# Optimization experiments

Measured on AMD Instinct MI355X. Metric: run time of the kernel, lower is better.

Reference implementation:

```python
import jax, jax.numpy as jnp
import numpy as np

C_S = 384; C_Z = 256; HD = 16; NH = 12; NQ = 4; NV = 8; L = 512
WC = float(np.sqrt(2.0 / (9.0 * NQ)))
WL = float(np.sqrt(1.0 / 3.0))


def quat2rot(q):
    # q: [L,4] -> R: [L,3,3] (normalized quaternion to rotation matrix)
    q = q / jnp.linalg.norm(q, axis=-1, keepdims=True)
    w, x, y, z = q[..., 0], q[..., 1], q[..., 2], q[..., 3]
    R = jnp.stack([
        1 - 2 * (y * y + z * z), 2 * (x * y - w * z), 2 * (x * z + w * y),
        2 * (x * y + w * z), 1 - 2 * (x * x + z * z), 2 * (y * z - w * x),
        2 * (x * z - w * y), 2 * (y * z + w * x), 1 - 2 * (x * x + y * y)
    ], axis=-1)
    return R.reshape(q.shape[:-1] + (3, 3))


def _layer_norm(x, g, b, eps=1e-5):
    m = x.mean(-1, keepdims=True)
    v = x.var(-1, keepdims=True)
    return (x - m) / jnp.sqrt(v + eps) * g + b


def setup_inputs() -> dict:
    key = jax.random.key(0)
    ks = jax.random.split(key, 20)
    f32 = jnp.float32
    def w(k, shape, fan_in):
        return (jax.random.normal(k, shape) / np.sqrt(fan_in)).astype(f32)
    shid = NH * (C_Z + HD + NV * 3 + NV)  # 3648
    return {
        "s": jax.random.normal(ks[0], (1, L, C_S), f32),
        "z": jax.random.normal(ks[1], (1, L, L, C_Z), f32),
        "quat_tns": jax.random.normal(ks[2], (1, L, 4), f32),
        "trsl_tns": jax.random.normal(ks[3], (1, L, 3), f32),
        "Wq": w(ks[4], (C_S, NH * HD), C_S),
        "Wk": w(ks[5], (C_S, NH * HD), C_S),
        "Wv": w(ks[6], (C_S, NH * HD), C_S),
        "Wqp": w(ks[7], (C_S, NH * NQ * 3), C_S),
        "Wkp": w(ks[8], (C_S, NH * NQ * 3), C_S),
        "Wvp": w(ks[9], (C_S, NH * NV * 3), C_S),
        "Wb": w(ks[10], (C_Z, NH), C_Z),
        "Ws": w(ks[11], (shid, C_S), shid),
        "bs": jnp.zeros((C_S,), f32),
        "scale": jnp.full((NH,), np.log(np.e - 1.0), f32),
        "g1": jnp.ones((C_S,), f32), "b1": jnp.zeros((C_S,), f32),
        "Wm1": w(ks[12], (C_S, C_S), C_S), "bm1": jnp.zeros((C_S,), f32),
        "Wm2": w(ks[13], (C_S, C_S), C_S), "bm2": jnp.zeros((C_S,), f32),
        "Wm3": w(ks[14], (C_S, C_S), C_S), "bm3": jnp.zeros((C_S,), f32),
        "g2": jnp.ones((C_S,), f32), "b2": jnp.zeros((C_S,), f32),
    }


def reference(s, z, quat_tns, trsl_tns, Wq, Wk, Wv, Wqp, Wkp, Wvp, Wb, Ws, bs,
              scale, g1, b1, Wm1, bm1, Wm2, bm2, Wm3, bm3, g2, b2):
    N, Lr, _ = s.shape
    q = (s @ Wq).reshape(N, Lr, NH, HD)
    k = (s @ Wk).reshape(N, Lr, NH, HD)
    v = (s @ Wv).reshape(N, Lr, NH, HD)
    qp = (s @ Wqp).reshape(N, Lr, NH, NQ, 3)
    kp = (s @ Wkp).reshape(N, Lr, NH, NQ, 3)
    vp = (s @ Wvp).reshape(N, Lr, NH, NV, 3)
    b = z @ Wb                                   # [N,L,L,H]
    R = quat2rot(quat_tns[0])[None]              # [1,L,3,3]
    t = trsl_tns[:, :, None, None, :]            # [1,L,1,1,3]

    def fwd_trans(x):                            # global frame: R x + t
        return jnp.einsum('nlij,nlhpj->nlhpi', R, x) + t

    qpp = fwd_trans(qp)                          # [N,L,H,Q,3]
    kpp = fwd_trans(kp)
    vpp = fwd_trans(vp)                          # [N,L,H,V,3]

    # sum over points and coords of squared distances -> [N,L,L,H]
    d2 = jnp.sum((qpp[:, :, None] - kpp[:, None, :]) ** 2, axis=(-1, -2))
    qk = jnp.einsum('nihd,njhd->nijh', q, k) / np.sqrt(HD)
    qkp = 0.5 * WC * jax.nn.softplus(scale)[None, None, None, :] * d2
    a = jax.nn.softmax(WL * (qk + b - qkp), axis=2)  # softmax over keys j

    op = jnp.einsum('nijh,nijc->nihc', a, z)         # [N,L,H,C_Z]
    ov = jnp.einsum('nijh,njhd->nihd', a, v)         # [N,L,H,HD]
    ovp_g = jnp.einsum('nijh,njhp->nihp', a, vpp.reshape(N, Lr, NH, NV * 3))
    ovp_g = ovp_g.reshape(N, Lr, NH, NV, 3)
    # inverse transform: R^T (y - t)
    ovp = jnp.einsum('nlji,nlhvj->nlhvi', R, ovp_g - t)
    ovp_norm = jnp.linalg.norm(ovp, axis=-1)         # [N,L,H,V]

    shid = jnp.concatenate(
        [op, ov, ovp.reshape(N, Lr, NH, NV * 3), ovp_norm], axis=3
    ).reshape(N, Lr, -1)
    s1 = _layer_norm(s + shid @ Ws + bs, g1, b1)
    h = jax.nn.relu(s1 @ Wm1 + bm1)
    h = jax.nn.relu(h @ Wm2 + bm2)
    h = h @ Wm3 + bm3
    return _layer_norm(s1 + h, g2, b2)
```

## Files before the change

### kernel.cpp

```cpp
#include <hip/hip_runtime.h>
#include <math.h>

#define LSEQ 512
#define CS 384
#define CZ 256
#define HD 16
#define NH 12
#define NQ 4
#define NV 8
#define NALL 1152
#define SHID 3648
#define OFF_Q 0
#define OFF_K 192
#define OFF_V 384
#define OFF_QP 576
#define OFF_KP 720
#define OFF_VP 864

#define WC_CONST 0.2357022603955158f
#define WL_CONST 0.5773502691896258f

typedef __attribute__((ext_vector_type(8))) short bf16x8;
typedef __attribute__((ext_vector_type(4))) float f32x4;

__device__ __forceinline__ short f2bf(float f) {
  unsigned u = __builtin_bit_cast(unsigned, f);
  unsigned r = (u + 0x7FFF + ((u >> 16) & 1)) >> 16;
  return (short)r;
}

__global__ void k_prep(const float* quat, const float* trsl, const float* scale,
                       const float* Wb, float* R, float* T, float* CH,
                       unsigned short* WBP) {
  int t = threadIdx.x;
  if (t < LSEQ) {
    float w = quat[t*4+0], x = quat[t*4+1], y = quat[t*4+2], z = quat[t*4+3];
    float inv = 1.0f / sqrtf(w*w + x*x + y*y + z*z);
    w *= inv; x *= inv; y *= inv; z *= inv;
    float* r = R + t*9;
    r[0] = 1.f - 2.f*(y*y + z*z); r[1] = 2.f*(x*y - w*z);       r[2] = 2.f*(x*z + w*y);
    r[3] = 2.f*(x*y + w*z);       r[4] = 1.f - 2.f*(x*x + z*z); r[5] = 2.f*(y*z - w*x);
    r[6] = 2.f*(x*z - w*y);       r[7] = 2.f*(y*z + w*x);       r[8] = 1.f - 2.f*(x*x + y*y);
    T[t*3+0] = trsl[t*3+0]; T[t*3+1] = trsl[t*3+1]; T[t*3+2] = trsl[t*3+2];
  }
  if (t < NH) {
    float sc = scale[t];
    float sp = (sc > 20.f) ? sc : logf(1.f + expf(sc));
    CH[t] = 0.5f * WC_CONST * sp;
  }
  if (t < CZ) {
    #pragma unroll
    for (int h = 0; h < 16; h++)
      WBP[t*16 + h] = (h < NH) ? (unsigned short)f2bf(Wb[t*NH + h]) : (unsigned short)0;
  }
}

__global__ void k_concat(const float* Wq, const float* Wk, const float* Wv,
                         const float* Wqp, const float* Wkp, const float* Wvp,
                         float* Wcat) {
  int idx = blockIdx.x * 256 + threadIdx.x;
  if (idx >= CS * NALL) return;
  int r = idx / NALL, c = idx % NALL;
  float v;
  if (c < 192)       v = Wq [r*192 + c];
  else if (c < 384)  v = Wk [r*192 + (c-192)];
  else if (c < 576)  v = Wv [r*192 + (c-384)];
  else if (c < 720)  v = Wqp[r*144 + (c-576)];
  else if (c < 864)  v = Wkp[r*144 + (c-720)];
  else               v = Wvp[r*288 + (c-864)];
  Wcat[idx] = v;
}

__global__ __launch_bounds__(256) void k_gemm(
    const float* A, const float* B, float* C, const float* bias,
    int K, int lda, int ldb, int ldc, int splitk, int relu, int reluA) {
  int ks = blockIdx.z;
  int Ksub = K / splitk;
  int kbeg = ks * Ksub, kend = kbeg + Ksub;

  __shared__ __align__(16) float As[16][68];
  __shared__ __align__(16) float Bs[16][68];
  int t = threadIdx.x;
  int m0 = blockIdx.y * 64, n0 = blockIdx.x * 64;
  int arow = t >> 2,  akq = (t & 3) * 4;
  int bkk  = t >> 4,  bnq = (t & 15) * 4;
  int ty = (t >> 4) * 4, tx = (t & 15) * 4;
  float acc[4][4];
  #pragma unroll
  for (int r = 0; r < 4; r++)
    #pragma unroll
    for (int c = 0; c < 4; c++) acc[r][c] = 0.f;

  const float* aptr  = A + (long)(m0 + arow) * lda + akq;
  const float* bbase = B + n0 + bnq;
  float4 av = *(const float4*)&aptr[kbeg];
  float4 bv = *(const float4*)&bbase[(long)(kbeg + bkk) * ldb];

  for (int kb = kbeg; kb < kend; kb += 16) {
    float4 a_cur = av, b_cur = bv;
    if (reluA) {
      a_cur.x = fmaxf(a_cur.x, 0.f); a_cur.y = fmaxf(a_cur.y, 0.f);
      a_cur.z = fmaxf(a_cur.z, 0.f); a_cur.w = fmaxf(a_cur.w, 0.f);
    }
    __syncthreads();
    As[akq+0][arow] = a_cur.x; As[akq+1][arow] = a_cur.y;
    As[akq+2][arow] = a_cur.z; As[akq+3][arow] = a_cur.w;
    *(float4*)&Bs[bkk][bnq] = b_cur;
    __syncthreads();
    if (kb + 16 < kend) {
      av = *(const float4*)&aptr[kb + 16];
      bv = *(const float4*)&bbase[(long)(kb + 16 + bkk) * ldb];
    }
    #pragma unroll
    for (int kk = 0; kk < 16; kk++) {
      float4 a4 = *(float4*)&As[kk][ty];
      float4 b4 = *(float4*)&Bs[kk][tx];
      acc[0][0] += a4.x*b4.x; acc[0][1] += a4.x*b4.y; acc[0][2] += a4.x*b4.z; acc[0][3] += a4.x*b4.w;
      acc[1][0] += a4.y*b4.x; acc[1][1] += a4.y*b4.y; acc[1][2] += a4.y*b4.z; acc[1][3] += a4.y*b4.w;
      acc[2][0] += a4.z*b4.x; acc[2][1] += a4.z*b4.y; acc[2][2] += a4.z*b4.z; acc[2][3] += a4.z*b4.w;
      acc[3][0] += a4.w*b4.x; acc[3][1] += a4.w*b4.y; acc[3][2] += a4.w*b4.z; acc[3][3] += a4.w*b4.w;
    }
  }

  if (splitk == 1) {
    #pragma unroll
    for (int r = 0; r < 4; r++) {
      int m = m0 + ty + r;
      #pragma unroll
      for (int c = 0; c < 4; c++) {
        int n = n0 + tx + c;
        float v = acc[r][c] + (bias ? bias[n] : 0.f);
        if (relu) v = fmaxf(v, 0.f);
        C[(long)m * ldc + n] = v;
      }
    }
  } else {
    #pragma unroll
    for (int r = 0; r < 4; r++) {
      int m = m0 + ty + r;
      #pragma unroll
      for (int c = 0; c < 4; c++) {
        int n = n0 + tx + c;
        float v = acc[r][c] + ((ks == 0 && bias) ? bias[n] : 0.f);
        atomicAdd(&C[(long)m * ldc + n], v);
      }
    }
  }
}

__global__ void k_trans(const float* P, const float* R, const float* T,
                        float* QPP, float* KT, float* KPT, float* VBT) {
  int task = blockIdx.y;
  int idx = blockIdx.x * 256 + threadIdx.x;
  if (idx >= LSEQ * NH) return;
  int h = idx / LSEQ, l = idx % LSEQ;
  const float* r = R + l*9;
  float t0 = T[l*3], t1 = T[l*3+1], t2 = T[l*3+2];
  const float* prow = P + (long)l * NALL;
  if (task == 0) {
    #pragma unroll
    for (int pq = 0; pq < NQ; pq++) {
      const float* x = prow + OFF_QP + h*12 + pq*3;
      float a = x[0], b = x[1], c = x[2];
      float* o = QPP + l*144 + h*12 + pq*3;
      o[0] = r[0]*a + r[1]*b + r[2]*c + t0;
      o[1] = r[3]*a + r[4]*b + r[5]*c + t1;
      o[2] = r[6]*a + r[7]*b + r[8]*c + t2;
    }
    #pragma unroll
    for (int d = 0; d < HD; d++)
      KT[(h*HD + d)*LSEQ + l] = prow[OFF_K + h*HD + d];
  } else if (task == 1) {
    #pragma unroll
    for (int pq = 0; pq < NQ; pq++) {
      const float* x = prow + OFF_KP + h*12 + pq*3;
      float a = x[0], b = x[1], c = x[2];
      KPT[(h*12 + pq*3 + 0)*LSEQ + l] = r[0]*a + r[1]*b + r[2]*c + t0;
      KPT[(h*12 + pq*3 + 1)*LSEQ + l] = r[3]*a + r[4]*b + r[5]*c + t1;
      KPT[(h*12 + pq*3 + 2)*LSEQ + l] = r[6]*a + r[7]*b + r[8]*c + t2;
    }
  } else {
    #pragma unroll
    for (int d = 0; d < 16; d++)
      VBT[((long)(h*40 + d))*LSEQ + l] = prow[OFF_V + h*16 + d];
    #pragma unroll
    for (int pv = 0; pv < NV; pv++) {
      const float* x = prow + OFF_VP + h*24 + pv*3;
      float a = x[0], b = x[1], c = x[2];
      VBT[((long)(h*40 + 16 + 3*pv + 0))*LSEQ + l] = r[0]*a + r[1]*b + r[2]*c + t0;
      VBT[((long)(h*40 + 16 + 3*pv + 1))*LSEQ + l] = r[3]*a + r[4]*b + r[5]*c + t1;
      VBT[((long)(h*40 + 16 + 3*pv + 2))*LSEQ + l] = r[6]*a + r[7]*b + r[8]*c + t2;
    }
  }
}

__global__ __launch_bounds__(512) void k_logit(const float* P, const float* QPP,
    const float* KT, const float* KPT, const float* CH, float* LG) {
  int i = blockIdx.x;
  int j = threadIdx.x;
  #pragma unroll
  for (int h = 0; h < NH; h++) {
    float kreg[16];
    #pragma unroll
    for (int d = 0; d < 16; d++) kreg[d] = KT[(h*16 + d)*LSEQ + j];
    float kp[12];
    #pragma unroll
    for (int p = 0; p < 12; p++) kp[p] = KPT[(h*12 + p)*LSEQ + j];
    float ch = CH[h];
    const float* q  = P + (long)i*NALL + OFF_Q + h*HD;
    const float* qp = QPP + i*144 + h*12;
    float dot = 0.f;
    #pragma unroll
    for (int d = 0; d < 16; d++) dot += q[d] * kreg[d];
    float d2 = 0.f;
    #pragma unroll
    for (int p = 0; p < 12; p++) { float dd = qp[p] - kp[p]; d2 += dd*dd; }
    LG[((long)i*NH + h)*LSEQ + j] = WL_CONST * (0.25f*dot - ch*d2);
  }
}

__global__ __launch_bounds__(256) void k_fused(const float* zin,
    const unsigned short* WBP, const float* LG, const float* VBT,
    float* SH, float* OVT, float* SSUM) {
  __shared__ __align__(16) float lgs[NH][264];
  __shared__ __align__(16) float es[NH][68];
  __shared__ float sred[4][NH];
  int i = blockIdx.x, js = blockIdx.y, t = threadIdx.x;
  int jbase = js * 256;
  int w = t >> 6, l = t & 63;
  int r = l & 15, kg = l >> 4;

  const float* lgsrc = LG + (long)i * NH * LSEQ + jbase;
  #pragma unroll
  for (int idx = t; idx < NH*256/4; idx += 256) {
    int h = idx >> 6, q4 = idx & 63;
    *(float4*)&lgs[h][q4*4] = *(const float4*)&lgsrc[h*LSEQ + q4*4];
  }

  bf16x8 bfrag[8];
  #pragma unroll
  for (int kt = 0; kt < 8; kt++)
    #pragma unroll
    for (int jj = 0; jj < 8; jj++)
      bfrag[kt][jj] = (short)WBP[(kt*32 + kg*8 + jj)*16 + r];

  float accop[NH];
  #pragma unroll
  for (int h = 0; h < NH; h++) accop[h] = 0.f;
  int pair0 = t, pair1 = t + 256;
  int h0 = pair0 / 40;
  int h1 = pair1 / 40;
  float accv0 = 0.f, accv1 = 0.f;
  float sparts = 0.f;
  int hh = (r < NH) ? r : 0;

  __syncthreads();

  for (int jt = 0; jt < 256; jt += 64) {
    int j0 = jt + w*16;
    int j0g = jbase + j0;
    const float* zrow = zin + ((long)i*LSEQ + j0g + r)*CZ + kg*8;
    f32x4 acc = {0.f, 0.f, 0.f, 0.f};
    #pragma unroll
    for (int kt = 0; kt < 8; kt++) {
      float4 z0 = *(const float4*)(zrow + kt*32);
      float4 z1 = *(const float4*)(zrow + kt*32 + 4);
      bf16x8 af;
      af[0] = f2bf(z0.x); af[1] = f2bf(z0.y); af[2] = f2bf(z0.z); af[3] = f2bf(z0.w);
      af[4] = f2bf(z1.x); af[5] = f2bf(z1.y); af[6] = f2bf(z1.z); af[7] = f2bf(z1.w);
      acc = __builtin_amdgcn_mfma_f32_16x16x32_bf16(af, bfrag[kt], acc, 0, 0, 0);
    }
    float4 lgv = *(float4*)&lgs[hh][j0 + kg*4];
    float e0 = __expf(lgv.x + WL_CONST*acc[0]);
    float e1 = __expf(lgv.y + WL_CONST*acc[1]);
    float e2 = __expf(lgv.z + WL_CONST*acc[2]);
    float e3 = __expf(lgv.w + WL_CONST*acc[3]);
    if (r < NH) {
      sparts += e0 + e1 + e2 + e3;
      *(float4*)&es[r][w*16 + kg*4] = make_float4(e0, e1, e2, e3);
    }
    __syncthreads();
    const float* zc = zin + ((long)i*LSEQ + jbase + jt)*CZ + t;
    #pragma unroll 4
    for (int jj = 0; jj < 64; jj += 4) {
      float z0 = zc[(jj+0)*CZ], z1 = zc[(jj+1)*CZ];
      float z2 = zc[(jj+2)*CZ], z3 = zc[(jj+3)*CZ];
      #pragma unroll
      for (int h = 0; h < NH; h++) {
        float4 ev = *(float4*)&es[h][jj];
        accop[h] += ev.x*z0 + ev.y*z1 + ev.z*z2 + ev.w*z3;
      }
    }
    {
      const float* vb0 = VBT + ((long)pair0)*LSEQ + jbase + jt;
      #pragma unroll
      for (int jj = 0; jj < 64; jj += 4) {
        float4 vv = *(const float4*)&vb0[jj];
        float4 ev = *(float4*)&es[h0][jj];
        accv0 += vv.x*ev.x + vv.y*ev.y + vv.z*ev.z + vv.w*ev.w;
      }
      if (pair1 < 480) {
        const float* vb1 = VBT + ((long)pair1)*LSEQ + jbase + jt;
        #pragma unroll
        for (int jj = 0; jj < 64; jj += 4) {
          float4 vv = *(const float4*)&vb1[jj];
          float4 ev = *(float4*)&es[h1][jj];
          accv1 += vv.x*ev.x + vv.y*ev.y + vv.z*ev.z + vv.w*ev.w;
        }
      }
    }
    __syncthreads();
  }

  sparts += __shfl_xor(sparts, 16);
  sparts += __shfl_xor(sparts, 32);
  if (l < NH) sred[w][l] = sparts;
  __syncthreads();
  if (t < NH)
    atomicAdd(&SSUM[i*16 + t], sred[0][t] + sred[1][t] + sred[2][t] + sred[3][t]);

  float* sh = SH + (long)i * SHID + t;
  #pragma unroll
  for (int h = 0; h < NH; h++) atomicAdd(&sh[h * 304], accop[h]);
  atomicAdd(&OVT[(long)i*480 + pair0], accv0);
  if (pair1 < 480) atomicAdd(&OVT[(long)i*480 + pair1], accv1);
}

__global__ __launch_bounds__(256) void k_opnorm(const float* SSUM, float* SH) {
  int i = blockIdx.x, t = threadIdx.x;
  float* sh = SH + (long)i * SHID + t;
  #pragma unroll
  for (int h = 0; h < NH; h++) {
    float inv = 1.0f / SSUM[i*16 + h];
    sh[h * 304] *= inv;
  }
}

__global__ void k_ovp(const float* OVT, const float* SSUM, const float* R,
                      const float* T, float* SH) {
  int idx = blockIdx.x * 256 + threadIdx.x;
  if (idx >= LSEQ * NH) return;
  int l = idx / NH, h = idx % NH;
  float inv = 1.0f / SSUM[l*16 + h];
  const float* o = OVT + (long)l*480 + h*40;
  float* sh = SH + (long)l * SHID + h * 304;
  #pragma unroll
  for (int d = 0; d < 16; d++) sh[256 + d] = o[d] * inv;
  const float* r = R + l*9;
  float t0 = T[l*3], t1 = T[l*3+1], t2 = T[l*3+2];
  #pragma unroll
  for (int v = 0; v < NV; v++) {
    float a = o[16+3*v+0]*inv - t0, b = o[16+3*v+1]*inv - t1, c = o[16+3*v+2]*inv - t2;
    float x = r[0]*a + r[3]*b + r[6]*c;
    float y = r[1]*a + r[4]*b + r[7]*c;
    float zz= r[2]*a + r[5]*b + r[8]*c;
    sh[272 + 3*v + 0] = x;
    sh[272 + 3*v + 1] = y;
    sh[272 + 3*v + 2] = zz;
    sh[296 + v] = sqrtf(x*x + y*y + zz*zz);
  }
}

__global__ __launch_bounds__(384) void k_ln(const float* res, const float* y,
                                            const float* g, const float* b, float* out) {
  int l = blockIdx.x, t = threadIdx.x;
  __shared__ float red1[6], red2[6];
  __shared__ float mv[2];
  float x = res[(long)l * CS + t] + y[(long)l * CS + t];
  float s = x, s2 = x * x;
  #pragma unroll
  for (int off = 32; off >= 1; off >>= 1) { s += __shfl_xor(s, off); s2 += __shfl_xor(s2, off); }
  if ((t & 63) == 0) { red1[t >> 6] = s; red2[t >> 6] = s2; }
  __syncthreads();
  if (t == 0) {
    float ss = 0.f, ss2 = 0.f;
    #pragma unroll
    for (int u = 0; u < 6; u++) { ss += red1[u]; ss2 += red2[u]; }
    float m = ss / CS;
    float var = ss2 / CS - m * m;
    mv[0] = m; mv[1] = 1.0f / sqrtf(var + 1e-5f);
  }
  __syncthreads();
  out[(long)l * CS + t] = (x - mv[0]) * mv[1] * g[t] + b[t];
}

extern "C" void kernel_launch(void* const* d_in, const int* in_sizes, int n_in,
                              void* d_out, int out_size, void* d_ws, size_t ws_size,
                              hipStream_t stream) {
  const float* s    = (const float*)d_in[0];
  const float* z    = (const float*)d_in[1];
  const float* quat = (const float*)d_in[2];
  const float* trsl = (const float*)d_in[3];
  const float* Wq   = (const float*)d_in[4];
  const float* Wk   = (const float*)d_in[5];
  const float* Wv   = (const float*)d_in[6];
  const float* Wqp  = (const float*)d_in[7];
  const float* Wkp  = (const float*)d_in[8];
  const float* Wvp  = (const float*)d_in[9];
  const float* Wb   = (const float*)d_in[10];
  const float* Ws   = (const float*)d_in[11];
  const float* bs   = (const float*)d_in[12];
  const float* scale= (const float*)d_in[13];
  const float* g1   = (const float*)d_in[14];
  const float* b1   = (const float*)d_in[15];
  const float* Wm1  = (const float*)d_in[16];
  const float* bm1  = (const float*)d_in[17];
  const float* Wm2  = (const float*)d_in[18];
  const float* bm2  = (const float*)d_in[19];
  const float* Wm3  = (const float*)d_in[20];
  const float* bm3  = (const float*)d_in[21];
  const float* g2   = (const float*)d_in[22];
  const float* b2   = (const float*)d_in[23];
  float* out = (float*)d_out;

  float* p = (float*)d_ws;
  float* R    = p; p += 512*9;
  float* T    = p; p += 512*3;
  float* CH   = p; p += 16;
  unsigned short* WBP = (unsigned short*)p; p += (CZ*16)/2;
  float* Wcat = p; p += (long)CS*NALL;
  float* QPP  = p; p += LSEQ*144;
  float* KT   = p; p += NH*HD*LSEQ;
  float* KPT  = p; p += NH*12*LSEQ;
  float* VBT  = p; p += (long)NH*40*LSEQ;
  float* LG   = p; p += (long)LSEQ*NH*LSEQ;
  float* S1   = p; p += LSEQ*CS;
  float* ZB   = p;
  float* P    = p; p += (long)LSEQ*NALL;
  float* T1   = p; p += LSEQ*CS;
  float* H1   = p; p += LSEQ*CS;
  float* H2   = p; p += LSEQ*CS;
  float* H3   = p; p += LSEQ*CS;
  float* SH   = p; p += (long)LSEQ*SHID;
  float* OVT  = p; p += (long)LSEQ*480;
  float* SSUM = p; p += LSEQ*16;
  size_t zbytes = ((size_t)LSEQ*NALL + 4*LSEQ*CS + (size_t)LSEQ*SHID
                   + (size_t)LSEQ*480 + LSEQ*16) * sizeof(float);

  hipMemsetAsync(ZB, 0, zbytes, stream);
  k_prep<<<1, 512, 0, stream>>>(quat, trsl, scale, Wb, R, T, CH, WBP);
  k_concat<<<(CS*NALL + 255)/256, 256, 0, stream>>>(Wq, Wk, Wv, Wqp, Wkp, Wvp, Wcat);
  k_gemm<<<dim3(NALL/64, LSEQ/64, 2), 256, 0, stream>>>(
      s, Wcat, P, nullptr, CS, CS, NALL, NALL, 2, 0, 0);
  k_trans<<<dim3(24, 3), 256, 0, stream>>>(P, R, T, QPP, KT, KPT, VBT);
  k_logit<<<LSEQ, 512, 0, stream>>>(P, QPP, KT, KPT, CH, LG);
  k_fused<<<dim3(LSEQ, 2), 256, 0, stream>>>(z, WBP, LG, VBT, SH, OVT, SSUM);
  k_opnorm<<<LSEQ, 256, 0, stream>>>(SSUM, SH);
  k_ovp<<<(LSEQ*NH + 255)/256, 256, 0, stream>>>(OVT, SSUM, R, T, SH);
  k_gemm<<<dim3(CS/64, LSEQ/64, 12), 256, 0, stream>>>(
      SH, Ws, T1, bs, SHID, SHID, CS, CS, 12, 0, 0);
  k_ln<<<LSEQ, CS, 0, stream>>>(s, T1, g1, b1, S1);
  k_gemm<<<dim3(CS/64, LSEQ/64, 8), 256, 0, stream>>>(
      S1, Wm1, H1, bm1, CS, CS, CS, CS, 8, 0, 0);
  k_gemm<<<dim3(CS/64, LSEQ/64, 8), 256, 0, stream>>>(
      H1, Wm2, H2, bm2, CS, CS, CS, CS, 8, 0, 1);
  k_gemm<<<dim3(CS/64, LSEQ/64, 8), 256, 0, stream>>>(
      H2, Wm3, H3, bm3, CS, CS, CS, CS, 8, 0, 1);
  k_ln<<<LSEQ, CS, 0, stream>>>(S1, H3, g2, b2, out);
}
```

Measured before the change: 698.8 us.

## Use split-bf16 MFMA GEMMs and fuse logit computation into attention kernel

Replaces the fp32 SIMT tiled GEMM with an MFMA GEMM that splits the fp32 operands into high and low bf16 parts, doing three MFMAs per tile to keep near-fp32 accuracy. The weights are pre-transposed and split by a new conversion kernel, and split-K factors are changed. Separately, the logit kernel and its L×H×L intermediate buffer are removed, with logits now computed directly into shared memory inside the fused attention kernel. The intent is to use the matrix cores and to avoid writing and re-reading the large logit buffer. In exchange it adds a weight-conversion pass on every call and loads B fragments straight from global memory with no shared-memory reuse.

```diff
diff --git a/kernel.cpp b/kernel.cpp
--- a/kernel.cpp
+++ b/kernel.cpp
@@ -71,79 +71,108 @@
   Wcat[idx] = v;
 }
 
-__global__ __launch_bounds__(256) void k_gemm(
-    const float* A, const float* B, float* C, const float* bias,
-    int K, int lda, int ldb, int ldc, int splitk, int relu, int reluA) {
-  int ks = blockIdx.z;
+__global__ __launch_bounds__(256) void k_cvtall(
+    const float* Wcat, const float* Ws, const float* Wm1, const float* Wm2, const float* Wm3,
+    unsigned short* WcatH, unsigned short* WcatL,
+    unsigned short* WsH, unsigned short* WsL,
+    unsigned short* Wm1H, unsigned short* Wm1L,
+    unsigned short* Wm2H, unsigned short* Wm2L,
+    unsigned short* Wm3H, unsigned short* Wm3L) {
+  int tb = blockIdx.x;
+  const float* src; unsigned short *dh, *dl; int K, N, tile;
+  if (tb < 108)      { src=Wcat; dh=WcatH; dl=WcatL; K=384;  N=1152; tile=tb; }
+  else if (tb < 450) { src=Ws;   dh=WsH;   dl=WsL;   K=3648; N=384;  tile=tb-108; }
+  else if (tb < 486) { src=Wm1;  dh=Wm1H;  dl=Wm1L;  K=384;  N=384;  tile=tb-450; }
+  else if (tb < 522) { src=Wm2;  dh=Wm2H;  dl=Wm2L;  K=384;  N=384;  tile=tb-486; }
+  else               { src=Wm3;  dh=Wm3H;  dl=Wm3L;  K=384;  N=384;  tile=tb-522; }
+  int tN = N >> 6;
+  int k0 = (tile / tN) * 64, n0 = (tile % tN) * 64;
+  __shared__ float ts[64][65];
+  int t = threadIdx.x;
+  int cr = t & 63, rr = t >> 6;
+  #pragma unroll
+  for (int u = 0; u < 16; u++) {
+    int row = rr + u*4;
+    ts[row][cr] = src[(long)(k0+row)*N + n0 + cr];
+  }
+  __syncthreads();
+  #pragma unroll
+  for (int u = 0; u < 16; u++) {
+    int nr = rr + u*4;
+    float v = ts[cr][nr];
+    unsigned uv = __builtin_bit_cast(unsigned, v);
+    unsigned short h = (unsigned short)(uv >> 16);
+    float hf = __builtin_bit_cast(float, uv & 0xFFFF0000u);
+    float lf = v - hf;
+    unsigned short lo = (unsigned short)(__builtin_bit_cast(unsigned, lf) >> 16);
+    long o = (long)(n0+nr)*K + k0 + cr;
+    dh[o] = h; dl[o] = lo;
+  }
+}
+
+__global__ __launch_bounds__(256) void k_gemm_bb(
+    const float* A, const unsigned short* Bh, const unsigned short* Bl,
+    float* C, const float* bias, int K, int N, int splitk, int reluA) {
+  int t = threadIdx.x;
+  int w = t >> 6, lane = t & 63, r = lane & 15, kg = lane >> 4;
+  int m0 = blockIdx.y * 64 + w * 16;
+  int n0 = blockIdx.x * 64;
   int Ksub = K / splitk;
-  int kbeg = ks * Ksub, kend = kbeg + Ksub;
-
-  __shared__ __align__(16) float As[16][68];
-  __shared__ __align__(16) float Bs[16][68];
-  int t = threadIdx.x;
-  int m0 = blockIdx.y * 64, n0 = blockIdx.x * 64;
-  int arow = t >> 2,  akq = (t & 3) * 4;
-  int bkk  = t >> 4,  bnq = (t & 15) * 4;
-  int ty = (t >> 4) * 4, tx = (t & 15) * 4;
-  float acc[4][4];
-  #pragma unroll
-  for (int r = 0; r < 4; r++)
-    #pragma unroll
-    for (int c = 0; c < 4; c++) acc[r][c] = 0.f;
-
-  const float* aptr  = A + (long)(m0 + arow) * lda + akq;
-  const float* bbase = B + n0 + bnq;
-  float4 av = *(const float4*)&aptr[kbeg];
-  float4 bv = *(const float4*)&bbase[(long)(kbeg + bkk) * ldb];
-
-  for (int kb = kbeg; kb < kend; kb += 16) {
-    float4 a_cur = av, b_cur = bv;
+  int kbeg = blockIdx.z * Ksub, kend = kbeg + Ksub;
+
+  f32x4 acc[4];
+  #pragma unroll
+  for (int nt = 0; nt < 4; nt++) acc[nt] = (f32x4){0.f, 0.f, 0.f, 0.f};
+
+  const float* arow = A + (long)(m0 + r) * K + kg*8;
+  const unsigned short* bhp[4];
+  const unsigned short* blp[4];
+  #pragma unroll
+  for (int nt = 0; nt < 4; nt++) {
+    long off = (long)(n0 + nt*16 + r) * K + kg*8;
+    bhp[nt] = Bh + off;
+    blp[nt] = Bl + off;
+  }
+
+  for (int kc = kbeg; kc < kend; kc += 32) {
+    float4 a0 = *(const float4*)&arow[kc];
+    float4 a1 = *(const float4*)&arow[kc + 4];
     if (reluA) {
-      a_cur.x = fmaxf(a_cur.x, 0.f); a_cur.y = fmaxf(a_cur.y, 0.f);
-      a_cur.z = fmaxf(a_cur.z, 0.f); a_cur.w = fmaxf(a_cur.w, 0.f);
-    }
-    __syncthreads();
-    As[akq+0][arow] = a_cur.x; As[akq+1][arow] = a_cur.y;
-    As[akq+2][arow] = a_cur.z; As[akq+3][arow] = a_cur.w;
-    *(float4*)&Bs[bkk][bnq] = b_cur;
-    __syncthreads();
-    if (kb + 16 < kend) {
-      av = *(const float4*)&aptr[kb + 16];
-      bv = *(const float4*)&bbase[(long)(kb + 16 + bkk) * ldb];
-    }
-    #pragma unroll
-    for (int kk = 0; kk < 16; kk++) {
-      float4 a4 = *(float4*)&As[kk][ty];
-      float4 b4 = *(float4*)&Bs[kk][tx];
-      acc[0][0] += a4.x*b4.x; acc[0][1] += a4.x*b4.y; acc[0][2] += a4.x*b4.z; acc[0][3] += a4.x*b4.w;
-      acc[1][0] += a4.y*b4.x; acc[1][1] += a4.y*b4.y; acc[1][2] += a4.y*b4.z; acc[1][3] += a4.y*b4.w;
-      acc[2][0] += a4.z*b4.x; acc[2][1] += a4.z*b4.y; acc[2][2] += a4.z*b4.z; acc[2][3] += a4.z*b4.w;
-      acc[3][0] += a4.w*b4.x; acc[3][1] += a4.w*b4.y; acc[3][2] += a4.w*b4.z; acc[3][3] += a4.w*b4.w;
-    }
-  }
-
-  if (splitk == 1) {
-    #pragma unroll
-    for (int r = 0; r < 4; r++) {
-      int m = m0 + ty + r;
-      #pragma unroll
-      for (int c = 0; c < 4; c++) {
-        int n = n0 + tx + c;
-        float v = acc[r][c] + (bias ? bias[n] : 0.f);
-        if (relu) v = fmaxf(v, 0.f);
-        C[(long)m * ldc + n] = v;
-      }
-    }
-  } else {
-    #pragma unroll
-    for (int r = 0; r < 4; r++) {
-      int m = m0 + ty + r;
-      #pragma unroll
-      for (int c = 0; c < 4; c++) {
-        int n = n0 + tx + c;
-        float v = acc[r][c] + ((ks == 0 && bias) ? bias[n] : 0.f);
-        atomicAdd(&C[(long)m * ldc + n], v);
-      }
+      a0.x = fmaxf(a0.x, 0.f); a0.y = fmaxf(a0.y, 0.f);
+      a0.z = fmaxf(a0.z, 0.f); a0.w = fmaxf(a0.w, 0.f);
+      a1.x = fmaxf(a1.x, 0.f); a1.y = fmaxf(a1.y, 0.f);
+      a1.z = fmaxf(a1.z, 0.f); a1.w = fmaxf(a1.w, 0.f);
+    }
+    float av[8] = {a0.x, a0.y, a0.z, a0.w, a1.x, a1.y, a1.z, a1.w};
+    bf16x8 ah, al;
+    #pragma unroll
+    for (int e = 0; e < 8; e++) {
+      unsigned uv = __builtin_bit_cast(unsigned, av[e]);
+      ah[e] = (short)(uv >> 16);
+      float hf = __builtin_bit_cast(float, uv & 0xFFFF0000u);
+      al[e] = (short)(__builtin_bit_cast(unsigned, av[e] - hf) >> 16);
+    }
+    #pragma unroll
+    for (int nt = 0; nt < 4; nt++) {
+      bf16x8 bh = *(const bf16x8*)&bhp[nt][kc];
+      bf16x8 bl = *(const bf16x8*)&blp[nt][kc];
+      acc[nt] = __builtin_amdgcn_mfma_f32_16x16x32_bf16(ah, bh, acc[nt], 0, 0, 0);
+      acc[nt] = __builtin_amdgcn_mfma_f32_16x16x32_bf16(al, bh, acc[nt], 0, 0, 0);
+      acc[nt] = __builtin_amdgcn_mfma_f32_16x16x32_bf16(ah, bl, acc[nt], 0, 0, 0);
+    }
+  }
+
+  bool add_bias = (bias != nullptr) && (blockIdx.z == 0);
+  #pragma unroll
+  for (int nt = 0; nt < 4; nt++) {
+    int n = n0 + nt*16 + r;
+    float bv = add_bias ? bias[n] : 0.f;
+    #pragma unroll
+    for (int reg = 0; reg < 4; reg++) {
+      int m = m0 + kg*4 + reg;
+      float v = acc[nt][reg] + bv;
+      if (splitk == 1) C[(long)m * N + n] = v;
+      else atomicAdd(&C[(long)m * N + n], v);
     }
   }
 }
@@ -194,33 +223,9 @@
   }
 }
 
-__global__ __launch_bounds__(512) void k_logit(const float* P, const float* QPP,
-    const float* KT, const float* KPT, const float* CH, float* LG) {
-  int i = blockIdx.x;
-  int j = threadIdx.x;
-  #pragma unroll
-  for (int h = 0; h < NH; h++) {
-    float kreg[16];
-    #pragma unroll
-    for (int d = 0; d < 16; d++) kreg[d] = KT[(h*16 + d)*LSEQ + j];
-    float kp[12];
-    #pragma unroll
-    for (int p = 0; p < 12; p++) kp[p] = KPT[(h*12 + p)*LSEQ + j];
-    float ch = CH[h];
-    const float* q  = P + (long)i*NALL + OFF_Q + h*HD;
-    const float* qp = QPP + i*144 + h*12;
-    float dot = 0.f;
-    #pragma unroll
-    for (int d = 0; d < 16; d++) dot += q[d] * kreg[d];
-    float d2 = 0.f;
-    #pragma unroll
-    for (int p = 0; p < 12; p++) { float dd = qp[p] - kp[p]; d2 += dd*dd; }
-    LG[((long)i*NH + h)*LSEQ + j] = WL_CONST * (0.25f*dot - ch*d2);
-  }
-}
-
 __global__ __launch_bounds__(256) void k_fused(const float* zin,
-    const unsigned short* WBP, const float* LG, const float* VBT,
+    const unsigned short* WBP, const float* P, const float* QPP,
+    const float* KT, const float* KPT, const float* CH, const float* VBT,
     float* SH, float* OVT, float* SSUM) {
   __shared__ __align__(16) float lgs[NH][264];
   __shared__ __align__(16) float es[NH][68];
@@ -229,12 +234,31 @@
   int jbase = js * 256;
   int w = t >> 6, l = t & 63;
   int r = l & 15, kg = l >> 4;
-
-  const float* lgsrc = LG + (long)i * NH * LSEQ + jbase;
-  #pragma unroll
-  for (int idx = t; idx < NH*256/4; idx += 256) {
-    int h = idx >> 6, q4 = idx & 63;
-    *(float4*)&lgs[h][q4*4] = *(const float4*)&lgsrc[h*LSEQ + q4*4];
+  int hh = (r < NH) ? r : 0;
+
+  {
+    int j = jbase + t;
+    const float* qb  = P + (long)i*NALL + OFF_Q;
+    const float* qpb = QPP + i*144;
+    #pragma unroll 2
+    for (int h = 0; h < NH; h++) {
+      float kreg[16];
+      #pragma unroll
+      for (int d = 0; d < 16; d++) kreg[d] = KT[(h*16 + d)*LSEQ + j];
+      float kp[12];
+      #pragma unroll
+      for (int p = 0; p < 12; p++) kp[p] = KPT[(h*12 + p)*LSEQ + j];
+      float ch = CH[h];
+      const float* q  = qb + h*HD;
+      const float* qp = qpb + h*12;
+      float dot = 0.f;
+      #pragma unroll
+      for (int d = 0; d < 16; d++) dot += q[d] * kreg[d];
+      float d2 = 0.f;
+      #pragma unroll
+      for (int p = 0; p < 12; p++) { float dd = qp[p] - kp[p]; d2 += dd*dd; }
+      lgs[h][t] = WL_CONST * (0.25f*dot - ch*d2);
+    }
   }
 
   bf16x8 bfrag[8];
@@ -248,11 +272,9 @@
   #pragma unroll
   for (int h = 0; h < NH; h++) accop[h] = 0.f;
   int pair0 = t, pair1 = t + 256;
-  int h0 = pair0 / 40;
-  int h1 = pair1 / 40;
+  int h0 = pair0 / 40, h1 = pair1 / 40;
   float accv0 = 0.f, accv1 = 0.f;
   float sparts = 0.f;
-  int hh = (r < NH) ? r : 0;
 
   __syncthreads();
 
@@ -419,11 +441,20 @@
   float* CH   = p; p += 16;
   unsigned short* WBP = (unsigned short*)p; p += (CZ*16)/2;
   float* Wcat = p; p += (long)CS*NALL;
+  unsigned short* WcatH = (unsigned short*)p; p += (CS*NALL)/2;
+  unsigned short* WcatL = (unsigned short*)p; p += (CS*NALL)/2;
+  unsigned short* WsH   = (unsigned short*)p; p += (SHID*CS)/2;
+  unsigned short* WsL   = (unsigned short*)p; p += (SHID*CS)/2;
+  unsigned short* Wm1H  = (unsigned short*)p; p += (CS*CS)/2;
+  unsigned short* Wm1L  = (unsigned short*)p; p += (CS*CS)/2;
+  unsigned short* Wm2H  = (unsigned short*)p; p += (CS*CS)/2;
+  unsigned short* Wm2L  = (unsigned short*)p; p += (CS*CS)/2;
+  unsigned short* Wm3H  = (unsigned short*)p; p += (CS*CS)/2;
+  unsigned short* Wm3L  = (unsigned short*)p; p += (CS*CS)/2;
   float* QPP  = p; p += LSEQ*144;
   float* KT   = p; p += NH*HD*LSEQ;
   float* KPT  = p; p += NH*12*LSEQ;
   float* VBT  = p; p += (long)NH*40*LSEQ;
-  float* LG   = p; p += (long)LSEQ*NH*LSEQ;
   float* S1   = p; p += LSEQ*CS;
   float* ZB   = p;
   float* P    = p; p += (long)LSEQ*NALL;
@@ -440,21 +471,23 @@
   hipMemsetAsync(ZB, 0, zbytes, stream);
   k_prep<<<1, 512, 0, stream>>>(quat, trsl, scale, Wb, R, T, CH, WBP);
   k_concat<<<(CS*NALL + 255)/256, 256, 0, stream>>>(Wq, Wk, Wv, Wqp, Wkp, Wvp, Wcat);
-  k_gemm<<<dim3(NALL/64, LSEQ/64, 2), 256, 0, stream>>>(
-      s, Wcat, P, nullptr, CS, CS, NALL, NALL, 2, 0, 0);
+  k_cvtall<<<558, 256, 0, stream>>>(Wcat, Ws, Wm1, Wm2, Wm3,
+      WcatH, WcatL, WsH, WsL, Wm1H, Wm1L, Wm2H, Wm2L, Wm3H, Wm3L);
+  k_gemm_bb<<<dim3(NALL/64, LSEQ/64, 4), 256, 0, stream>>>(
+      s, WcatH, WcatL, P, nullptr, CS, NALL, 4, 0);
   k_trans<<<dim3(24, 3), 256, 0, stream>>>(P, R, T, QPP, KT, KPT, VBT);
-  k_logit<<<LSEQ, 512, 0, stream>>>(P, QPP, KT, KPT, CH, LG);
-  k_fused<<<dim3(LSEQ, 2), 256, 0, stream>>>(z, WBP, LG, VBT, SH, OVT, SSUM);
+  k_fused<<<dim3(LSEQ, 2), 256, 0, stream>>>(
+      z, WBP, P, QPP, KT, KPT, CH, VBT, SH, OVT, SSUM);
   k_opnorm<<<LSEQ, 256, 0, stream>>>(SSUM, SH);
   k_ovp<<<(LSEQ*NH + 255)/256, 256, 0, stream>>>(OVT, SSUM, R, T, SH);
-  k_gemm<<<dim3(CS/64, LSEQ/64, 12), 256, 0, stream>>>(
-      SH, Ws, T1, bs, SHID, SHID, CS, CS, 12, 0, 0);
+  k_gemm_bb<<<dim3(CS/64, LSEQ/64, 6), 256, 0, stream>>>(
+      SH, WsH, WsL, T1, bs, SHID, CS, 6, 0);
   k_ln<<<LSEQ, CS, 0, stream>>>(s, T1, g1, b1, S1);
-  k_gemm<<<dim3(CS/64, LSEQ/64, 8), 256, 0, stream>>>(
-      S1, Wm1, H1, bm1, CS, CS, CS, CS, 8, 0, 0);
-  k_gemm<<<dim3(CS/64, LSEQ/64, 8), 256, 0, stream>>>(
-      H1, Wm2, H2, bm2, CS, CS, CS, CS, 8, 0, 1);
-  k_gemm<<<dim3(CS/64, LSEQ/64, 8), 256, 0, stream>>>(
-      H2, Wm3, H3, bm3, CS, CS, CS, CS, 8, 0, 1);
+  k_gemm_bb<<<dim3(CS/64, LSEQ/64, 4), 256, 0, stream>>>(
+      S1, Wm1H, Wm1L, H1, bm1, CS, CS, 4, 0);
+  k_gemm_bb<<<dim3(CS/64, LSEQ/64, 4), 256, 0, stream>>>(
+      H1, Wm2H, Wm2L, H2, bm2, CS, CS, 4, 1);
+  k_gemm_bb<<<dim3(CS/64, LSEQ/64, 4), 256, 0, stream>>>(
+      H2, Wm3H, Wm3L, H3, bm3, CS, CS, 4, 1);
   k_ln<<<LSEQ, CS, 0, stream>>>(S1, H3, g2, b2, out);
 }
```

Measured after the change: 639.6 us. 8.5% less time.
